# Kernel optimization log

Hardware: AMD Instinct MI355X
Metric: run time of the kernel (lower is better)

## Reference

```python
import jax, jax.numpy as jnp
import numpy as np

N, E, D_IN, D_OUT = 50000, 800000, 32, 64


def setup_inputs() -> dict:
    key = jax.random.key(0)
    k1, k2, k3 = jax.random.split(key, 3)
    x = jax.random.normal(k1, (N, D_IN), dtype=jnp.float32)
    edge_index = jax.random.randint(k2, (2, E), 0, N)
    W = jax.random.normal(k3, (D_IN, D_OUT), dtype=jnp.float32) / np.sqrt(D_IN).astype(np.float32)
    b = jnp.zeros((D_OUT,), dtype=jnp.float32)
    return {"x": x, "edge_index": edge_index, "W": W, "b": b}


def gcn_conv(x, edge_index, W, b):
    n = x.shape[0]
    loop = jnp.arange(n)
    src = jnp.concatenate([edge_index[0], loop])  # message sources (x_j)
    dst = jnp.concatenate([edge_index[1], loop])  # aggregation targets
    xw = x @ W  # [N, D_OUT]
    deg = jax.ops.segment_sum(jnp.ones(src.shape[0], dtype=xw.dtype), dst, num_segments=n)
    dinv = jnp.where(deg > 0, jax.lax.rsqrt(jnp.where(deg > 0, deg, 1.0)), 0.0)
    norm = dinv[src] * dinv[dst]  # [E+N]
    msg = xw[src] * norm[:, None]  # gather + scale
    out = jax.ops.segment_sum(msg, dst, num_segments=n)  # scatter-add aggregate
    return out + b


def reference(x, edge_index, W, b):
    h = jax.nn.relu(gcn_conv(x, edge_index, W, b))
    # InnerProductDecoder over given edges: sigmoid(<h_i, h_j>)
    logits = jnp.sum(h[edge_index[0]] * h[edge_index[1]], axis=-1)  # [E]
    adj_pred = jax.nn.sigmoid(logits) + 1e-15
    return (adj_pred, edge_index)
```

## Files before the change

### kernel.cpp

```cpp
#include <hip/hip_runtime.h>
#include <hip/hip_fp8.h>

#define D_IN 32
#define D_OUT 64
#define NBMAX 800
#define BIN_BLKS 128
#define COPY_BLKS 784
#define CAP 32
#define BCAP 1280

__device__ __forceinline__ unsigned char f2fp8(float f) {
    __hip_fp8_e4m3 v(f);
    return (unsigned char)v.__x;
}
__device__ __forceinline__ float fp82f(unsigned char u) {
    __hip_fp8_e4m3 v;
    v.__x = (__hip_fp8_storage_t)u;
    return (float)v;
}
__device__ __forceinline__ float dot4fp8(unsigned int ua, unsigned int ub) {
    float s = 0.f;
#pragma unroll
    for (int k = 0; k < 4; ++k) {
        __hip_fp8_e4m3 fa, fb;
        fa.__x = (__hip_fp8_storage_t)(unsigned char)(ua >> (8 * k));
        fb.__x = (__hip_fp8_storage_t)(unsigned char)(ub >> (8 * k));
        s += (float)fa * (float)fb;
    }
    return s;
}

__global__ void __launch_bounds__(256) k_bin(const int* __restrict__ src,
                                             const int* __restrict__ dst,
                                             int* __restrict__ cellcnt,
                                             int* __restrict__ cells,
                                             const int* __restrict__ ei,
                                             float* __restrict__ outE,
                                             const float* __restrict__ x,
                                             const float* __restrict__ W,
                                             unsigned char* __restrict__ xws,
                                             int N, int E, int NB, int chunk) {
    int t = threadIdx.x;
    if (blockIdx.x >= BIN_BLKS) {
        int cb = blockIdx.x - BIN_BLKS;
        __shared__ float Ws[D_IN * D_OUT];
        __shared__ float xs[64 * D_IN];
        int node0 = cb * 64;
        for (int i = t; i < D_IN * D_OUT; i += 256) Ws[i] = W[i];
        for (int i = t; i < 64 * (D_IN / 4); i += 256) {
            int r = i >> 3, q = i & 7;
            int node = node0 + r;
            float4 v = make_float4(0.f, 0.f, 0.f, 0.f);
            if (node < N) v = *(const float4*)(x + (size_t)node * D_IN + q * 4);
            *(float4*)(xs + r * D_IN + q * 4) = v;
        }
        __syncthreads();
#pragma unroll
        for (int i = 0; i < 16; ++i) {
            int idx = i * 256 + t;
            int ln = idx >> 6, c = idx & 63;
            int node = node0 + ln;
            if (node < N) {
                float s = 0.f;
#pragma unroll
                for (int k = 0; k < D_IN; ++k) s += xs[ln * D_IN + k] * Ws[k * D_OUT + c];
                xws[(size_t)node * D_OUT + c] = f2fp8(s);
            }
        }
        int ct = cb * 256 + t;
        int cstride = COPY_BLKS * 256;
        int n4 = (2 * E) >> 2;
        const int4* ei4 = (const int4*)ei;
        float4* o4 = (float4*)outE;
        for (int i = ct; i < n4; i += cstride) {
            int4 v = ei4[i];
            o4[i] = make_float4((float)v.x, (float)v.y, (float)v.z, (float)v.w);
        }
        for (int i = n4 * 4 + ct; i < 2 * E; i += cstride) outE[i] = (float)ei[i];
        return;
    }
    __shared__ int cur[NBMAX];
    int blk = blockIdx.x;
    int s0 = blk * chunk;
    int s1 = s0 + chunk; if (s1 > E) s1 = E;
    for (int i = t; i < NB; i += 256) cur[i] = 0;
    __syncthreads();
    if (s0 < E) {
        for (int k = s0 + t * 8; k < s1; k += 2048) {
            if (k + 7 < s1) {
                int4 sa = *(const int4*)(src + k);
                int4 sb = *(const int4*)(src + k + 4);
                int4 da = *(const int4*)(dst + k);
                int4 db = *(const int4*)(dst + k + 4);
                int s8[8] = {sa.x, sa.y, sa.z, sa.w, sb.x, sb.y, sb.z, sb.w};
                int d8[8] = {da.x, da.y, da.z, da.w, db.x, db.y, db.z, db.w};
#pragma unroll
                for (int u = 0; u < 8; ++u) {
                    int d = d8[u], bin = d >> 6;
                    int pos = atomicAdd(&cur[bin], 1);
                    if (pos < CAP)
                        cells[((size_t)bin * BIN_BLKS + blk) * CAP + pos] = (s8[u] << 6) | (d & 63);
                }
            } else {
                for (int e = k; e < s1; ++e) {
                    int d = dst[e], bin = d >> 6;
                    int pos = atomicAdd(&cur[bin], 1);
                    if (pos < CAP)
                        cells[((size_t)bin * BIN_BLKS + blk) * CAP + pos] = (src[e] << 6) | (d & 63);
                }
            }
        }
    }
    __syncthreads();
    for (int i = t; i < NB; i += 256) cellcnt[(size_t)blk * NB + i] = min(cur[i], CAP);
}

__global__ void __launch_bounds__(256) k_build(const int* __restrict__ cellcnt,
                                               const int* __restrict__ cells,
                                               float* __restrict__ dinv,
                                               int* __restrict__ offs, int* __restrict__ ends,
                                               int* __restrict__ srcs,
                                               int N, int NB) {
    __shared__ int ebuf[BIN_BLKS * CAP];
    __shared__ int ccnt[BIN_BLKS], coff[BIN_BLKS + 1];
    __shared__ int lcnt[64], lofs[65], lcur[64];
    int bin = blockIdx.x, t = threadIdx.x;
    int node0 = bin * 64;
    if (t < 64) { lcnt[t] = 0; lcur[t] = 0; }
    if (t < BIN_BLKS) ccnt[t] = cellcnt[(size_t)t * NB + bin];
    __syncthreads();
    if (t == 0) {
        int r = 0;
#pragma unroll
        for (int i = 0; i < BIN_BLKS; ++i) { coff[i] = r; r += ccnt[i]; }
        coff[BIN_BLKS] = r;
    }
    __syncthreads();
    const int* crow = cells + (size_t)bin * BIN_BLKS * CAP;
#pragma unroll
    for (int i = 0; i < (BIN_BLKS * CAP) / 256; ++i) {
        int idx = i * 256 + t;
        int cell = idx >> 5, pos = idx & (CAP - 1);
        if (pos < ccnt[cell]) {
            int p = crow[idx];
            ebuf[coff[cell] + pos] = p;
            atomicAdd(&lcnt[p & 63], 1);
        }
    }
    __syncthreads();
    int ns = coff[BIN_BLKS];
    if (t == 0) {
        int r = 0;
#pragma unroll
        for (int i = 0; i < 64; ++i) { lofs[i] = r; r += lcnt[i]; }
        lofs[64] = r;
    }
    __syncthreads();
    int binbase = bin * BCAP;
    if (t < 64) {
        int node = node0 + t;
        if (node < N) {
            dinv[node] = rsqrtf((float)(lcnt[t] + 1));
            offs[node] = binbase + lofs[t];
            ends[node] = binbase + lofs[t + 1];
        }
    }
    __syncthreads();
    for (int k = t; k < ns; k += 256) {
        int p = ebuf[k];
        int d = p & 63;
        int slot = atomicAdd(&lcur[d], 1);
        srcs[binbase + lofs[d] + slot] = p >> 6;
    }
}

__global__ void k_agg(const unsigned char* __restrict__ xws, const float* __restrict__ dinv,
                      const int* __restrict__ offs, const int* __restrict__ ends,
                      const int* __restrict__ srcs,
                      const float* __restrict__ b, unsigned char* __restrict__ h, int n) {
    int g = blockIdx.x * blockDim.x + threadIdx.x;
    int d = g >> 6, c = g & 63;
    if (d >= n) return;
    float dd = dinv[d];
    float a0 = fp82f(xws[(size_t)d * D_OUT + c]) * dd;
    float a1 = 0.f, a2 = 0.f, a3 = 0.f;
    int kend = ends[d];
    for (int k = offs[d]; k < kend; k += 8) {
        int s[8];
        float v[8], w[8];
#pragma unroll
        for (int u = 0; u < 8; ++u) {
            int t = k + u;
            s[u] = srcs[t < kend ? t : kend - 1];
        }
#pragma unroll
        for (int u = 0; u < 8; ++u) {
            float xv = fp82f(xws[(size_t)s[u] * D_OUT + c]);
            w[u] = dinv[s[u]];
            v[u] = (k + u < kend) ? xv : 0.f;
        }
        a0 += v[0] * w[0]; a1 += v[1] * w[1]; a2 += v[2] * w[2]; a3 += v[3] * w[3];
        a0 += v[4] * w[4]; a1 += v[5] * w[5]; a2 += v[6] * w[6]; a3 += v[7] * w[7];
    }
    float r = dd * ((a0 + a1) + (a2 + a3)) + b[c];
    h[(size_t)d * D_OUT + c] = f2fp8(r > 0.f ? r : 0.f);
}

__global__ void k_decode(const int* __restrict__ e0, const int* __restrict__ e1,
                         const unsigned char* __restrict__ h, float* __restrict__ out,
                         int E, int halfE) {
    int g = blockIdx.x * blockDim.x + threadIdx.x;
    int pair = g >> 1, q = g & 1;
    if (pair >= halfE) return;
    int ea = pair;
    int eb = pair + halfE;
    bool hasB = eb < E;
    int ia = e0[ea], ja = e1[ea];
    int ib = hasB ? e0[eb] : ia;
    int jb = hasB ? e1[eb] : ja;
    const uint4* hia = (const uint4*)(h + (size_t)ia * D_OUT + q * 32);
    const uint4* hja = (const uint4*)(h + (size_t)ja * D_OUT + q * 32);
    const uint4* hib = (const uint4*)(h + (size_t)ib * D_OUT + q * 32);
    const uint4* hjb = (const uint4*)(h + (size_t)jb * D_OUT + q * 32);
    uint4 a0 = hia[0], a1 = hia[1];
    uint4 b0 = hja[0], b1 = hja[1];
    uint4 c0 = hib[0], c1 = hib[1];
    uint4 d0 = hjb[0], d1 = hjb[1];
    float pa = dot4fp8(a0.x, b0.x) + dot4fp8(a0.y, b0.y)
             + dot4fp8(a0.z, b0.z) + dot4fp8(a0.w, b0.w)
             + dot4fp8(a1.x, b1.x) + dot4fp8(a1.y, b1.y)
             + dot4fp8(a1.z, b1.z) + dot4fp8(a1.w, b1.w);
    float pb = dot4fp8(c0.x, d0.x) + dot4fp8(c0.y, d0.y)
             + dot4fp8(c0.z, d0.z) + dot4fp8(c0.w, d0.w)
             + dot4fp8(c1.x, d1.x) + dot4fp8(c1.y, d1.y)
             + dot4fp8(c1.z, d1.z) + dot4fp8(c1.w, d1.w);
    pa += __shfl_xor(pa, 1, 64);
    pb += __shfl_xor(pb, 1, 64);
    if (q == 0) {
        out[ea] = 1.0f / (1.0f + expf(-pa)) + 1e-15f;
        if (hasB) out[eb] = 1.0f / (1.0f + expf(-pb)) + 1e-15f;
    }
}

extern "C" void kernel_launch(void* const* d_in, const int* in_sizes, int n_in,
                              void* d_out, int out_size, void* d_ws, size_t ws_size,
                              hipStream_t stream) {
    const float* x = (const float*)d_in[0];
    const int*   ei = (const int*)d_in[1];
    const float* W = (const float*)d_in[2];
    const float* b = (const float*)d_in[3];

    const int N = in_sizes[0] / D_IN;
    const int E = in_sizes[1] / 2;
    const size_t NF = (size_t)N * D_OUT;
    const int NB = (N + 63) >> 6;

    float* out = (float*)d_out;

    char* base = (char*)d_ws;
    unsigned char*  xws     = (unsigned char*)base;
    unsigned char*  h       = (unsigned char*)(base + NF);
    float*          dinv    = (float*)(base + NF * 2);
    int*            offs    = (int*)(base + NF * 2 + (size_t)N * 4);
    int*            ends    = offs + N;
    int*            cellcnt = ends + N;
    int*            srcs    = cellcnt + (size_t)BIN_BLKS * NB;
    int*            cells   = srcs + (size_t)NB * BCAP;

    const int* srcv = ei;
    const int* dstv = ei + E;

    const int B = 256;
    const int gNF = (int)((NF + B - 1) / B);
    const int halfE = (E + 1) / 2;
    const int gD  = (int)(((long long)halfE * 2 + B - 1) / B);
    const int chunk = ((E + BIN_BLKS - 1) / BIN_BLKS + 7) & ~7;

    k_bin   <<<BIN_BLKS + COPY_BLKS, B, 0, stream>>>(srcv, dstv, cellcnt, cells,
                                                     ei, out + E, x, W, xws, N, E, NB, chunk);
    k_build <<<NB,  B, 0, stream>>>(cellcnt, cells, dinv, offs, ends, srcs, N, NB);
    k_agg   <<<gNF, B, 0, stream>>>(xws, dinv, offs, ends, srcs, b, h, N);
    k_decode<<<gD,  B, 0, stream>>>(srcv, dstv, h, out, E, halfE);
}
```

Baseline: 75.53 us.

## Fuse CSR build and aggregation into one per-bin kernel with global degree atomics

Merges the bin-build and aggregation kernels so each 512-thread block sorts its bin's edges into shared memory and aggregates its 64 nodes directly, with no global srcs/offs/dinv arrays. Source-node degrees are now computed by global atomics in the binning kernel (after a memset), and rsqrt is applied on the fly per gathered neighbour. This removes a kernel launch and the global CSR write/read round trip. In exchange it adds 800K global atomics, recomputes rsqrt per gather, and launches only about 782 blocks for aggregation, which may lower parallelism.

```diff
diff --git a/kernel.cpp b/kernel.cpp
--- a/kernel.cpp
+++ b/kernel.cpp
@@ -7,7 +7,6 @@
 #define BIN_BLKS 128
 #define COPY_BLKS 784
 #define CAP 32
-#define BCAP 1280
 
 __device__ __forceinline__ unsigned char f2fp8(float f) {
     __hip_fp8_e4m3 v(f);
@@ -32,6 +31,7 @@
 
 __global__ void __launch_bounds__(256) k_bin(const int* __restrict__ src,
                                              const int* __restrict__ dst,
+                                             int* __restrict__ deg,
                                              int* __restrict__ cellcnt,
                                              int* __restrict__ cells,
                                              const int* __restrict__ ei,
@@ -100,6 +100,7 @@
                     int pos = atomicAdd(&cur[bin], 1);
                     if (pos < CAP)
                         cells[((size_t)bin * BIN_BLKS + blk) * CAP + pos] = (s8[u] << 6) | (d & 63);
+                    atomicAdd(&deg[d], 1);
                 }
             } else {
                 for (int e = k; e < s1; ++e) {
@@ -107,6 +108,7 @@
                     int pos = atomicAdd(&cur[bin], 1);
                     if (pos < CAP)
                         cells[((size_t)bin * BIN_BLKS + blk) * CAP + pos] = (src[e] << 6) | (d & 63);
+                    atomicAdd(&deg[d], 1);
                 }
             }
         }
@@ -115,17 +117,20 @@
     for (int i = t; i < NB; i += 256) cellcnt[(size_t)blk * NB + i] = min(cur[i], CAP);
 }
 
-__global__ void __launch_bounds__(256) k_build(const int* __restrict__ cellcnt,
-                                               const int* __restrict__ cells,
-                                               float* __restrict__ dinv,
-                                               int* __restrict__ offs, int* __restrict__ ends,
-                                               int* __restrict__ srcs,
-                                               int N, int NB) {
+__global__ void __launch_bounds__(512) k_ba(const unsigned char* __restrict__ xws,
+                                            const int* __restrict__ deg,
+                                            const int* __restrict__ cellcnt,
+                                            const int* __restrict__ cells,
+                                            const float* __restrict__ b,
+                                            unsigned char* __restrict__ h,
+                                            int N, int NB) {
     __shared__ int ebuf[BIN_BLKS * CAP];
+    __shared__ int sSrc[BIN_BLKS * CAP];
     __shared__ int ccnt[BIN_BLKS], coff[BIN_BLKS + 1];
     __shared__ int lcnt[64], lofs[65], lcur[64];
     int bin = blockIdx.x, t = threadIdx.x;
     int node0 = bin * 64;
+    float bc = b[t & 63];
     if (t < 64) { lcnt[t] = 0; lcur[t] = 0; }
     if (t < BIN_BLKS) ccnt[t] = cellcnt[(size_t)t * NB + bin];
     __syncthreads();
@@ -138,8 +143,8 @@
     __syncthreads();
     const int* crow = cells + (size_t)bin * BIN_BLKS * CAP;
 #pragma unroll
-    for (int i = 0; i < (BIN_BLKS * CAP) / 256; ++i) {
-        int idx = i * 256 + t;
+    for (int i = 0; i < (BIN_BLKS * CAP) / 512; ++i) {
+        int idx = i * 512 + t;
         int cell = idx >> 5, pos = idx & (CAP - 1);
         if (pos < ccnt[cell]) {
             int p = crow[idx];
@@ -156,54 +161,41 @@
         lofs[64] = r;
     }
     __syncthreads();
-    int binbase = bin * BCAP;
-    if (t < 64) {
-        int node = node0 + t;
-        if (node < N) {
-            dinv[node] = rsqrtf((float)(lcnt[t] + 1));
-            offs[node] = binbase + lofs[t];
-            ends[node] = binbase + lofs[t + 1];
-        }
-    }
-    __syncthreads();
-    for (int k = t; k < ns; k += 256) {
+    for (int k = t; k < ns; k += 512) {
         int p = ebuf[k];
         int d = p & 63;
         int slot = atomicAdd(&lcur[d], 1);
-        srcs[binbase + lofs[d] + slot] = p >> 6;
-    }
-}
-
-__global__ void k_agg(const unsigned char* __restrict__ xws, const float* __restrict__ dinv,
-                      const int* __restrict__ offs, const int* __restrict__ ends,
-                      const int* __restrict__ srcs,
-                      const float* __restrict__ b, unsigned char* __restrict__ h, int n) {
-    int g = blockIdx.x * blockDim.x + threadIdx.x;
-    int d = g >> 6, c = g & 63;
-    if (d >= n) return;
-    float dd = dinv[d];
-    float a0 = fp82f(xws[(size_t)d * D_OUT + c]) * dd;
-    float a1 = 0.f, a2 = 0.f, a3 = 0.f;
-    int kend = ends[d];
-    for (int k = offs[d]; k < kend; k += 8) {
-        int s[8];
-        float v[8], w[8];
-#pragma unroll
-        for (int u = 0; u < 8; ++u) {
-            int t = k + u;
-            s[u] = srcs[t < kend ? t : kend - 1];
-        }
-#pragma unroll
-        for (int u = 0; u < 8; ++u) {
-            float xv = fp82f(xws[(size_t)s[u] * D_OUT + c]);
-            w[u] = dinv[s[u]];
-            v[u] = (k + u < kend) ? xv : 0.f;
-        }
-        a0 += v[0] * w[0]; a1 += v[1] * w[1]; a2 += v[2] * w[2]; a3 += v[3] * w[3];
-        a0 += v[4] * w[4]; a1 += v[5] * w[5]; a2 += v[6] * w[6]; a3 += v[7] * w[7];
-    }
-    float r = dd * ((a0 + a1) + (a2 + a3)) + b[c];
-    h[(size_t)d * D_OUT + c] = f2fp8(r > 0.f ? r : 0.f);
+        sSrc[lofs[d] + slot] = p >> 6;
+    }
+    __syncthreads();
+    int w = t >> 6, c = t & 63;
+    for (int ln = w; ln < 64; ln += 8) {
+        int node = node0 + ln;
+        if (node >= N) continue;
+        float dd = rsqrtf((float)(lcnt[ln] + 1));
+        float a0 = fp82f(xws[(size_t)node * D_OUT + c]) * dd;
+        float a1 = 0.f, a2 = 0.f, a3 = 0.f;
+        int k0 = lofs[ln], k1 = lofs[ln + 1];
+        for (int k = k0; k < k1; k += 8) {
+            int s[8];
+            float v[8], wg[8];
+#pragma unroll
+            for (int u = 0; u < 8; ++u) {
+                int tt = k + u;
+                s[u] = sSrc[tt < k1 ? tt : k1 - 1];
+            }
+#pragma unroll
+            for (int u = 0; u < 8; ++u) {
+                float xv = fp82f(xws[(size_t)s[u] * D_OUT + c]);
+                wg[u] = rsqrtf((float)(deg[s[u]] + 1));
+                v[u] = (k + u < k1) ? xv : 0.f;
+            }
+            a0 += v[0] * wg[0]; a1 += v[1] * wg[1]; a2 += v[2] * wg[2]; a3 += v[3] * wg[3];
+            a0 += v[4] * wg[4]; a1 += v[5] * wg[5]; a2 += v[6] * wg[6]; a3 += v[7] * wg[7];
+        }
+        float r = dd * ((a0 + a1) + (a2 + a3)) + bc;
+        h[(size_t)node * D_OUT + c] = f2fp8(r > 0.f ? r : 0.f);
+    }
 }
 
 __global__ void k_decode(const int* __restrict__ e0, const int* __restrict__ e1,
@@ -260,25 +252,21 @@
     char* base = (char*)d_ws;
     unsigned char*  xws     = (unsigned char*)base;
     unsigned char*  h       = (unsigned char*)(base + NF);
-    float*          dinv    = (float*)(base + NF * 2);
-    int*            offs    = (int*)(base + NF * 2 + (size_t)N * 4);
-    int*            ends    = offs + N;
-    int*            cellcnt = ends + N;
-    int*            srcs    = cellcnt + (size_t)BIN_BLKS * NB;
-    int*            cells   = srcs + (size_t)NB * BCAP;
+    int*            deg     = (int*)(base + NF * 2);
+    int*            cellcnt = deg + N;
+    int*            cells   = cellcnt + (size_t)BIN_BLKS * NB;
 
     const int* srcv = ei;
     const int* dstv = ei + E;
 
     const int B = 256;
-    const int gNF = (int)((NF + B - 1) / B);
     const int halfE = (E + 1) / 2;
     const int gD  = (int)(((long long)halfE * 2 + B - 1) / B);
     const int chunk = ((E + BIN_BLKS - 1) / BIN_BLKS + 7) & ~7;
 
-    k_bin   <<<BIN_BLKS + COPY_BLKS, B, 0, stream>>>(srcv, dstv, cellcnt, cells,
+    hipMemsetAsync(deg, 0, (size_t)N * 4, stream);
+    k_bin   <<<BIN_BLKS + COPY_BLKS, B, 0, stream>>>(srcv, dstv, deg, cellcnt, cells,
                                                      ei, out + E, x, W, xws, N, E, NB, chunk);
-    k_build <<<NB,  B, 0, stream>>>(cellcnt, cells, dinv, offs, ends, srcs, N, NB);
-    k_agg   <<<gNF, B, 0, stream>>>(xws, dinv, offs, ends, srcs, b, h, N);
+    k_ba    <<<NB,  512, 0, stream>>>(xws, deg, cellcnt, cells, b, h, N, NB);
     k_decode<<<gD,  B, 0, stream>>>(srcv, dstv, h, out, E, halfE);
 }
```

Result: slower. 124.7 us (+65.0%).
